# Kernel tuning notes

Hardware: AMD Instinct MI355X
Metric: run time of the kernel (lower is better)

## Reference

```python
import jax, jax.numpy as jnp
import numpy as np

IN_FEATS, N_HIDDEN, N_CLASSES = 128, 256, 32
N0, N1, B = 614400, 40960, 4096
F0, F1 = 15, 10
BN_EPS = 1e-5


def setup_inputs() -> dict:
    key = jax.random.key(0)
    ks = jax.random.split(key, 20)
    s = 0.02
    inp = {
        "x": jax.random.uniform(ks[0], (N0, IN_FEATS), jnp.float32) * 10.0,
        "nbr0": jax.random.randint(ks[1], (N1, F0), 0, N0, jnp.int32),
        "nbr1": jax.random.randint(ks[2], (B, F1), 0, N1, jnp.int32),
        # layer0: SAGEConv(128->256, 'pool')
        "W_pool": jax.random.normal(ks[3], (IN_FEATS, IN_FEATS), jnp.float32) * s,
        "b_pool": jnp.zeros((IN_FEATS,), jnp.float32),
        "W_self0": jax.random.normal(ks[4], (N_HIDDEN, IN_FEATS), jnp.float32) * s,
        "W_neigh0": jax.random.normal(ks[5], (N_HIDDEN, IN_FEATS), jnp.float32) * s,
        "b0": jnp.zeros((N_HIDDEN,), jnp.float32),
        # BatchNorm1d(n_hidden)
        "gamma0": jnp.ones((N_HIDDEN,), jnp.float32),
        "beta0": jnp.zeros((N_HIDDEN,), jnp.float32),
        # layer1: SAGEConv(256->32, 'lstm'); torch LSTM gate order i,f,g,o
        "W_ih": jax.random.normal(ks[6], (4 * N_HIDDEN, N_HIDDEN), jnp.float32) * s,
        "W_hh": jax.random.normal(ks[7], (4 * N_HIDDEN, N_HIDDEN), jnp.float32) * s,
        "b_ih": jnp.zeros((4 * N_HIDDEN,), jnp.float32),
        "b_hh": jnp.zeros((4 * N_HIDDEN,), jnp.float32),
        "W_self1": jax.random.normal(ks[8], (N_CLASSES, N_HIDDEN), jnp.float32) * s,
        "W_neigh1": jax.random.normal(ks[9], (N_CLASSES, N_HIDDEN), jnp.float32) * s,
        "b1": jnp.zeros((N_CLASSES,), jnp.float32),
    }
    return inp


def _lstm_agg(seq, W_ih, W_hh, b_ih, b_hh):
    # seq: [B, K, H]; run LSTM over K neighbor steps, return final hidden [B, H]
    Bsz, _, H = seq.shape
    xs = jnp.swapaxes(seq, 0, 1)  # [K, B, H]

    def step(carry, x_t):
        h_t, c_t = carry
        g = x_t @ W_ih.T + b_ih + h_t @ W_hh.T + b_hh  # [B, 4H]
        i, f, gg, o = jnp.split(g, 4, axis=-1)
        c = jax.nn.sigmoid(f) * c_t + jax.nn.sigmoid(i) * jnp.tanh(gg)
        h = jax.nn.sigmoid(o) * jnp.tanh(c)
        return (h, c), None

    init = (jnp.zeros((Bsz, H), seq.dtype), jnp.zeros((Bsz, H), seq.dtype))
    (hT, _), _ = jax.lax.scan(step, init, xs)
    return hT


def reference(x, nbr0, nbr1, W_pool, b_pool, W_self0, W_neigh0, b0,
              gamma0, beta0, W_ih, W_hh, b_ih, b_hh, W_self1, W_neigh1, b1):
    n1 = nbr0.shape[0]
    b = nbr1.shape[0]
    h = jnp.log(x + 1.0)  # [N0, in_feats]

    # --- layer 0: SAGEConv 'pool' ---
    hp = jax.nn.relu(h @ W_pool.T + b_pool)           # [N0, in_feats]
    h_neigh = jnp.max(hp[nbr0], axis=1)               # [N1, in_feats]
    h0 = h[:n1] @ W_self0.T + h_neigh @ W_neigh0.T + b0  # [N1, n_hidden]

    # BN (training stats) + relu (dropout p=0)
    mu = jnp.mean(h0, axis=0)
    var = jnp.var(h0, axis=0)
    h0 = (h0 - mu) * jax.lax.rsqrt(var + BN_EPS) * gamma0 + beta0
    h0 = jax.nn.relu(h0)

    # --- layer 1: SAGEConv 'lstm' ---
    seq = h0[nbr1]                                    # [B, F1, n_hidden]
    h_neigh1 = _lstm_agg(seq, W_ih, W_hh, b_ih, b_hh)  # [B, n_hidden]
    out = h0[:b] @ W_self1.T + h_neigh1 @ W_neigh1.T + b1  # [B, n_classes]
    return out
```

## Files before the change

### kernel.cpp

```cpp
#include <hip/hip_runtime.h>

#define N0v 614400
#define N1v 40960
#define BATCHv 4096

typedef __attribute__((ext_vector_type(8))) short short8;
typedef __attribute__((ext_vector_type(4))) float floatx4;

static __device__ __forceinline__ float flog1p(float v) { return __logf(v + 1.0f); }
static __device__ __forceinline__ float sigf(float v) { return 1.0f / (1.0f + __expf(-v)); }
static __device__ __forceinline__ float tanhfast(float v) {
    return 1.0f - 2.0f / (__expf(2.0f * v) + 1.0f);
}
static __device__ __forceinline__ unsigned short f2bf(float f) {
    union { float f; unsigned u; } v; v.f = f;
    unsigned r = v.u + 0x7FFFu + ((v.u >> 16) & 1u);
    return (unsigned short)(r >> 16);
}
static __device__ __forceinline__ float bf2f(unsigned short u) {
    return __uint_as_float(((unsigned)u) << 16);
}

__global__ __launch_bounds__(256) void cvt_weights_kernel(
    const float* __restrict__ Wp, const float* __restrict__ Ws0,
    const float* __restrict__ Wn0, const float* __restrict__ Wih,
    const float* __restrict__ Whh, const float* __restrict__ bih,
    const float* __restrict__ bhh,
    unsigned short* __restrict__ Wpb, unsigned short* __restrict__ Ws0b,
    unsigned short* __restrict__ Wn0b, unsigned short* __restrict__ Wihb,
    unsigned short* __restrict__ Whhb, float* __restrict__ bsum)
{
    const int g = blockIdx.x * 256 + threadIdx.x;
    if (g < 16384)            Wpb[g] = f2bf(Wp[g]);
    else if (g < 49152)       Ws0b[g - 16384] = f2bf(Ws0[g - 16384]);
    else if (g < 81920)       Wn0b[g - 49152] = f2bf(Wn0[g - 49152]);
    else if (g < 344064)      Wihb[g - 81920] = f2bf(Wih[g - 81920]);
    else if (g < 606208)      Whhb[g - 344064] = f2bf(Whh[g - 344064]);
    else if (g < 607232) { const int i = g - 606208; bsum[i] = bih[i] + bhh[i]; }
}

__global__ __launch_bounds__(256) void pool_max_kernel(
    const float* __restrict__ x, const int* __restrict__ nbr0,
    const unsigned short* __restrict__ Wpb, const float* __restrict__ bp,
    unsigned short* __restrict__ hnb)
{
    __shared__ unsigned short smem[64 * 72 + 128 * 72];
    __shared__ unsigned red[512];
    __shared__ int nodes[64];
    unsigned short* aT = smem;
    unsigned short* wT = smem + 64 * 72;

    const int tid = threadIdx.x;
    const size_t base = (size_t)blockIdx.x * 60;
    if (tid < 64) nodes[tid] = (tid < 60) ? nbr0[base + tid] : 0;
    for (int i = tid; i < 512; i += 256) red[i] = 0u;

    const int lane = tid & 63, wv = tid >> 6;
    const int ml = lane & 15, q = lane >> 4, qk = q * 8;

    floatx4 acc[8];
#pragma unroll
    for (int ct = 0; ct < 8; ++ct) acc[ct] = (floatx4){0.f, 0.f, 0.f, 0.f};

    for (int kc = 0; kc < 2; ++kc) {
        __syncthreads();
        for (int i = tid; i < 512; i += 256) {
            const int row = i >> 3, seg = i & 7;
            short8 o = {0, 0, 0, 0, 0, 0, 0, 0};
            if (row < 60) {
                const float* s = x + (size_t)nodes[row] * 128 + kc * 64 + seg * 8;
                const float4 f0 = *(const float4*)s;
                const float4 f1 = *(const float4*)(s + 4);
                o[0] = (short)f2bf(flog1p(f0.x)); o[1] = (short)f2bf(flog1p(f0.y));
                o[2] = (short)f2bf(flog1p(f0.z)); o[3] = (short)f2bf(flog1p(f0.w));
                o[4] = (short)f2bf(flog1p(f1.x)); o[5] = (short)f2bf(flog1p(f1.y));
                o[6] = (short)f2bf(flog1p(f1.z)); o[7] = (short)f2bf(flog1p(f1.w));
            }
            *(short8*)&aT[row * 72 + seg * 8] = o;
        }
        for (int i = tid; i < 1024; i += 256) {
            const int row = i >> 3, seg = i & 7;
            *(short8*)&wT[row * 72 + seg * 8] =
                *(const short8*)&Wpb[(size_t)row * 128 + kc * 64 + seg * 8];
        }
        __syncthreads();
#pragma unroll
        for (int k0 = 0; k0 < 64; k0 += 32) {
            const short8 a = *(const short8*)&aT[(wv * 16 + ml) * 72 + k0 + qk];
#pragma unroll
            for (int ct = 0; ct < 8; ++ct) {
                const short8 b = *(const short8*)&wT[(ct * 16 + ml) * 72 + k0 + qk];
                acc[ct] = __builtin_amdgcn_mfma_f32_16x16x32_bf16(a, b, acc[ct], 0, 0, 0);
            }
        }
    }
    __syncthreads();
#pragma unroll
    for (int ct = 0; ct < 8; ++ct) {
        const int col = ct * 16 + ml;
        const float bb = bp[col];
#pragma unroll
        for (int r = 0; r < 4; ++r) {
            const int row = wv * 16 + q * 4 + r;
            if (row < 60) {
                const float v = fmaxf(acc[ct][r] + bb, 0.0f);
                atomicMax(&red[(row / 15) * 128 + col], __float_as_uint(v));
            }
        }
    }
    __syncthreads();
    for (int i = tid; i < 512; i += 256)
        hnb[(size_t)blockIdx.x * 512 + i] = f2bf(__uint_as_float(red[i]));
}

__global__ __launch_bounds__(256) void h0_kernel(
    const float* __restrict__ x, const unsigned short* __restrict__ hnb,
    const unsigned short* __restrict__ Ws0b, const unsigned short* __restrict__ Wn0b,
    const float* __restrict__ b0, unsigned short* __restrict__ h0bf,
    float* __restrict__ bn_sum, float* __restrict__ bn_sq)
{
    __shared__ unsigned short smem[64 * 72 + 128 * 72];
    unsigned short* aT = smem;
    unsigned short* wT = smem + 64 * 72;

    const int tid = threadIdx.x;
    const int m0 = blockIdx.x * 64, c0 = blockIdx.y * 128;
    const int lane = tid & 63, wv = tid >> 6;
    const int ml = lane & 15, q = lane >> 4, qk = q * 8;

    floatx4 acc[8];
#pragma unroll
    for (int ct = 0; ct < 8; ++ct) acc[ct] = (floatx4){0.f, 0.f, 0.f, 0.f};

    for (int kc = 0; kc < 4; ++kc) {
        __syncthreads();
        for (int i = tid; i < 512; i += 256) {
            const int row = i >> 3, seg = i & 7;
            const int k = kc * 64 + seg * 8;
            if (kc < 2) {
                const float* s = x + (size_t)(m0 + row) * 128 + k;
                const float4 f0 = *(const float4*)s;
                const float4 f1 = *(const float4*)(s + 4);
                short8 o;
                o[0] = (short)f2bf(flog1p(f0.x)); o[1] = (short)f2bf(flog1p(f0.y));
                o[2] = (short)f2bf(flog1p(f0.z)); o[3] = (short)f2bf(flog1p(f0.w));
                o[4] = (short)f2bf(flog1p(f1.x)); o[5] = (short)f2bf(flog1p(f1.y));
                o[6] = (short)f2bf(flog1p(f1.z)); o[7] = (short)f2bf(flog1p(f1.w));
                *(short8*)&aT[row * 72 + seg * 8] = o;
            } else {
                *(short8*)&aT[row * 72 + seg * 8] =
                    *(const short8*)&hnb[(size_t)(m0 + row) * 128 + (k - 128)];
            }
        }
        for (int i = tid; i < 1024; i += 256) {
            const int row = i >> 3, seg = i & 7;
            const int k = kc * 64 + seg * 8;
            const size_t cg = (size_t)(c0 + row);
            *(short8*)&wT[row * 72 + seg * 8] = (kc < 2)
                ? *(const short8*)&Ws0b[cg * 128 + k]
                : *(const short8*)&Wn0b[cg * 128 + (k - 128)];
        }
        __syncthreads();
#pragma unroll
        for (int k0 = 0; k0 < 64; k0 += 32) {
            const short8 a = *(const short8*)&aT[(wv * 16 + ml) * 72 + k0 + qk];
#pragma unroll
            for (int ct = 0; ct < 8; ++ct) {
                const short8 b = *(const short8*)&wT[(ct * 16 + ml) * 72 + k0 + qk];
                acc[ct] = __builtin_amdgcn_mfma_f32_16x16x32_bf16(a, b, acc[ct], 0, 0, 0);
            }
        }
    }
    __syncthreads();
    float* scr = (float*)smem;
#pragma unroll
    for (int ct = 0; ct < 8; ++ct) {
        const int col = ct * 16 + ml, cg = c0 + col;
        const float bb = b0[cg];
        float s = 0.f, sq = 0.f;
#pragma unroll
        for (int r = 0; r < 4; ++r) {
            const int row = wv * 16 + q * 4 + r;
            const float v = acc[ct][r] + bb;
            h0bf[(size_t)(m0 + row) * 256 + cg] = f2bf(v);
            s += v; sq += v * v;
        }
        scr[(wv * 4 + q) * 128 + col] = s;
        scr[2048 + (wv * 4 + q) * 128 + col] = sq;
    }
    __syncthreads();
    if (tid < 128) {
        float s = 0.f, sq = 0.f;
#pragma unroll
        for (int j = 0; j < 16; ++j) {
            s += scr[j * 128 + tid];
            sq += scr[2048 + j * 128 + tid];
        }
        atomicAdd(&bn_sum[c0 + tid], s);
        atomicAdd(&bn_sq[c0 + tid], sq);
    }
}

__global__ void bn_stats_kernel(const float* __restrict__ bn_sum, const float* __restrict__ bn_sq,
                                const float* __restrict__ gamma, const float* __restrict__ beta,
                                float* __restrict__ scale, float* __restrict__ shift)
{
    const int c = threadIdx.x;
    const float inv_n = 1.0f / (float)N1v;
    const float mu = bn_sum[c] * inv_n;
    const float var = bn_sq[c] * inv_n - mu * mu;
    const float rs = rsqrtf(var + 1e-5f);
    const float sc = rs * gamma[c];
    scale[c] = sc;
    shift[c] = beta[c] - mu * sc;
}

__global__ __launch_bounds__(256) void bn_apply_kernel(
    const unsigned short* __restrict__ h0bf, const float* __restrict__ scale,
    const float* __restrict__ shift, unsigned short* __restrict__ h0nbf)
{
    const int gid = blockIdx.x * 256 + threadIdx.x;
    const int c0 = (gid * 8) & 255;
    const short8 v = *(const short8*)&h0bf[(size_t)gid * 8];
    short8 o;
#pragma unroll
    for (int j = 0; j < 8; ++j) {
        const float f = bf2f((unsigned short)v[j]);
        o[j] = (short)f2bf(fmaxf(fmaf(f, scale[c0 + j], shift[c0 + j]), 0.0f));
    }
    *(short8*)&h0nbf[(size_t)gid * 8] = o;
}

__global__ __launch_bounds__(256) void lstm_step_kernel(
    const unsigned short* __restrict__ h0nbf, const int* __restrict__ nbr1,
    const unsigned short* __restrict__ hbprev, const unsigned short* __restrict__ Wihb,
    const unsigned short* __restrict__ Whhb, const float* __restrict__ bsum,
    float* __restrict__ cst, unsigned short* __restrict__ hb, int t)
{
    __shared__ unsigned short smem[64 * 72 + 128 * 72];
    __shared__ int nodes[64];
    unsigned short* aT = smem;
    unsigned short* wT = smem + 64 * 72;

    const int tid = threadIdx.x;
    const int m0 = blockIdx.x * 64, c0h = blockIdx.y * 32;
    const int lane = tid & 63, wv = tid >> 6;
    const int ml = lane & 15, q = lane >> 4, qk = q * 8;

    if (tid < 64) nodes[tid] = nbr1[(size_t)(m0 + tid) * 10 + t];

    floatx4 acc[8];
#pragma unroll
    for (int ct = 0; ct < 8; ++ct) acc[ct] = (floatx4){0.f, 0.f, 0.f, 0.f};

    const int kcN = (t == 0) ? 4 : 8;
    for (int kc = 0; kc < kcN; ++kc) {
        __syncthreads();
        for (int i = tid; i < 512; i += 256) {
            const int row = i >> 3, seg = i & 7;
            const int k = kc * 64 + seg * 8;
            *(short8*)&aT[row * 72 + seg * 8] = (kc < 4)
                ? *(const short8*)&h0nbf[(size_t)nodes[row] * 256 + k]
                : *(const short8*)&hbprev[(size_t)(m0 + row) * 256 + (k - 256)];
        }
        for (int i = tid; i < 1024; i += 256) {
            const int row = i >> 3, seg = i & 7;
            const int k = kc * 64 + seg * 8;
            const size_t wr = (size_t)((row >> 5) * 256 + c0h + (row & 31));
            *(short8*)&wT[row * 72 + seg * 8] = (kc < 4)
                ? *(const short8*)&Wihb[wr * 256 + k]
                : *(const short8*)&Whhb[wr * 256 + (k - 256)];
        }
        __syncthreads();
#pragma unroll
        for (int k0 = 0; k0 < 64; k0 += 32) {
            const short8 a = *(const short8*)&aT[(wv * 16 + ml) * 72 + k0 + qk];
#pragma unroll
            for (int ct = 0; ct < 8; ++ct) {
                const short8 b = *(const short8*)&wT[(ct * 16 + ml) * 72 + k0 + qk];
                acc[ct] = __builtin_amdgcn_mfma_f32_16x16x32_bf16(a, b, acc[ct], 0, 0, 0);
            }
        }
    }
#pragma unroll
    for (int hg = 0; hg < 2; ++hg) {
        const int hcol = hg * 16 + ml;
        const float bi = bsum[c0h + hcol];
        const float bf_ = bsum[256 + c0h + hcol];
        const float bg = bsum[512 + c0h + hcol];
        const float bo = bsum[768 + c0h + hcol];
#pragma unroll
        for (int r = 0; r < 4; ++r) {
            const int row = wv * 16 + q * 4 + r;
            const size_t idx = (size_t)(m0 + row) * 256 + c0h + hcol;
            const float gi = acc[hg][r] + bi;
            const float gf = acc[2 + hg][r] + bf_;
            const float gg = acc[4 + hg][r] + bg;
            const float go = acc[6 + hg][r] + bo;
            float c = sigf(gi) * tanhfast(gg);
            if (t > 0) c += sigf(gf) * cst[idx];
            cst[idx] = c;
            hb[idx] = f2bf(sigf(go) * tanhfast(c));
        }
    }
}

__global__ __launch_bounds__(256) void out_kernel(
    const unsigned short* __restrict__ h0nbf, const unsigned short* __restrict__ hTb,
    const float* __restrict__ Ws1, const float* __restrict__ Wn1,
    const float* __restrict__ b1, float* __restrict__ out)
{
    const int gid = blockIdx.x * 256 + threadIdx.x;
    const int row = gid >> 5, c = gid & 31;
    const unsigned short* a0 = h0nbf + (size_t)row * 256;
    const unsigned short* a1 = hTb + (size_t)row * 256;
    const float* w0 = Ws1 + (size_t)c * 256;
    const float* w1 = Wn1 + (size_t)c * 256;
    float s = b1[c];
#pragma unroll 4
    for (int k8 = 0; k8 < 32; ++k8) {
        const short8 av = *(const short8*)&a0[k8 * 8];
        const short8 bv = *(const short8*)&a1[k8 * 8];
        const float4 wa0 = *(const float4*)&w0[k8 * 8];
        const float4 wa1 = *(const float4*)&w0[k8 * 8 + 4];
        const float4 wb0 = *(const float4*)&w1[k8 * 8];
        const float4 wb1 = *(const float4*)&w1[k8 * 8 + 4];
        s += bf2f((unsigned short)av[0]) * wa0.x + bf2f((unsigned short)av[1]) * wa0.y;
        s += bf2f((unsigned short)av[2]) * wa0.z + bf2f((unsigned short)av[3]) * wa0.w;
        s += bf2f((unsigned short)av[4]) * wa1.x + bf2f((unsigned short)av[5]) * wa1.y;
        s += bf2f((unsigned short)av[6]) * wa1.z + bf2f((unsigned short)av[7]) * wa1.w;
        s += bf2f((unsigned short)bv[0]) * wb0.x + bf2f((unsigned short)bv[1]) * wb0.y;
        s += bf2f((unsigned short)bv[2]) * wb0.z + bf2f((unsigned short)bv[3]) * wb0.w;
        s += bf2f((unsigned short)bv[4]) * wb1.x + bf2f((unsigned short)bv[5]) * wb1.y;
        s += bf2f((unsigned short)bv[6]) * wb1.z + bf2f((unsigned short)bv[7]) * wb1.w;
    }
    out[gid] = s;
}

extern "C" void kernel_launch(void* const* d_in, const int* in_sizes, int n_in,
                              void* d_out, int out_size, void* d_ws, size_t ws_size,
                              hipStream_t stream)
{
    const float* x        = (const float*)d_in[0];
    const int*   nbr0     = (const int*)d_in[1];
    const int*   nbr1     = (const int*)d_in[2];
    const float* W_pool   = (const float*)d_in[3];
    const float* b_pool   = (const float*)d_in[4];
    const float* W_self0  = (const float*)d_in[5];
    const float* W_neigh0 = (const float*)d_in[6];
    const float* b0       = (const float*)d_in[7];
    const float* gamma0   = (const float*)d_in[8];
    const float* beta0    = (const float*)d_in[9];
    const float* W_ih     = (const float*)d_in[10];
    const float* W_hh     = (const float*)d_in[11];
    const float* b_ih     = (const float*)d_in[12];
    const float* b_hh     = (const float*)d_in[13];
    const float* W_self1  = (const float*)d_in[14];
    const float* W_neigh1 = (const float*)d_in[15];
    const float* b1       = (const float*)d_in[16];
    float* out = (float*)d_out;

    char* ws = (char*)d_ws;
    unsigned short* h0bf  = (unsigned short*)(ws);
    unsigned short* hnb   = (unsigned short*)(ws + 20971520);
    unsigned short* h0nbf = (unsigned short*)(ws + 31457280);
    float*          cst   = (float*)(ws + 52428800);
    unsigned short* hb0   = (unsigned short*)(ws + 56623104);
    unsigned short* hb1   = (unsigned short*)(ws + 58720256);
    unsigned short* Wpb   = (unsigned short*)(ws + 60817408);
    unsigned short* Ws0b  = (unsigned short*)(ws + 60850176);
    unsigned short* Wn0b  = (unsigned short*)(ws + 60915712);
    unsigned short* Wihb  = (unsigned short*)(ws + 60981248);
    unsigned short* Whhb  = (unsigned short*)(ws + 61505536);
    float*          bsum  = (float*)(ws + 62029824);
    float*          bn_sum   = (float*)(ws + 62033920);
    float*          bn_sq    = (float*)(ws + 62034944);
    float*          bn_scale = (float*)(ws + 62035968);
    float*          bn_shift = (float*)(ws + 62036992);

    hipMemsetAsync(bn_sum, 0, 2048, stream);

    cvt_weights_kernel<<<2372, 256, 0, stream>>>(W_pool, W_self0, W_neigh0, W_ih, W_hh,
                                                 b_ih, b_hh, Wpb, Ws0b, Wn0b, Wihb, Whhb, bsum);
    pool_max_kernel<<<N1v / 4, 256, 0, stream>>>(x, nbr0, Wpb, b_pool, hnb);
    h0_kernel<<<dim3(N1v / 64, 2), 256, 0, stream>>>(x, hnb, Ws0b, Wn0b, b0,
                                                     h0bf, bn_sum, bn_sq);
    bn_stats_kernel<<<1, 256, 0, stream>>>(bn_sum, bn_sq, gamma0, beta0, bn_scale, bn_shift);
    bn_apply_kernel<<<(N1v * 256 / 8) / 256, 256, 0, stream>>>(h0bf, bn_scale, bn_shift, h0nbf);

    for (int t = 0; t < 10; ++t) {
        const unsigned short* hp = (t & 1) ? hb1 : hb0;
        unsigned short*       hn = (t & 1) ? hb0 : hb1;
        lstm_step_kernel<<<dim3(BATCHv / 64, 8), 256, 0, stream>>>(
            h0nbf, nbr1, hp, Wihb, Whhb, bsum, cst, hn, t);
    }
    out_kernel<<<(BATCHv * 32) / 256, 256, 0, stream>>>(h0nbf, hb0, W_self1, W_neigh1, b1, out);
}
```

Measured before the change: 777.1 us.

## Fuse BN apply and LSTM steps into one cooperative persistent kernel

Replaces the BN-apply kernel and the ten per-timestep LSTM launches with a single cooperative kernel. A grid-wide sync separates the BN-apply phase from the LSTM phase and each timestep from the next. The aim is to remove eleven kernel launch gaps and tail effects. In exchange, the kernel now pays grid-barrier costs and is limited to 512 co-resident blocks, and the launch fails if those blocks cannot all be resident.

```diff
diff --git a/kernel.cpp b/kernel.cpp
--- a/kernel.cpp
+++ b/kernel.cpp
@@ -1,4 +1,7 @@
 #include <hip/hip_runtime.h>
+#include <hip/hip_cooperative_groups.h>
+
+namespace cg = cooperative_groups;
 
 #define N0v 614400
 #define N1v 40960
@@ -215,28 +218,16 @@
     shift[c] = beta[c] - mu * sc;
 }
 
-__global__ __launch_bounds__(256) void bn_apply_kernel(
-    const unsigned short* __restrict__ h0bf, const float* __restrict__ scale,
-    const float* __restrict__ shift, unsigned short* __restrict__ h0nbf)
-{
-    const int gid = blockIdx.x * 256 + threadIdx.x;
-    const int c0 = (gid * 8) & 255;
-    const short8 v = *(const short8*)&h0bf[(size_t)gid * 8];
-    short8 o;
-#pragma unroll
-    for (int j = 0; j < 8; ++j) {
-        const float f = bf2f((unsigned short)v[j]);
-        o[j] = (short)f2bf(fmaxf(fmaf(f, scale[c0 + j], shift[c0 + j]), 0.0f));
-    }
-    *(short8*)&h0nbf[(size_t)gid * 8] = o;
-}
-
-__global__ __launch_bounds__(256) void lstm_step_kernel(
-    const unsigned short* __restrict__ h0nbf, const int* __restrict__ nbr1,
-    const unsigned short* __restrict__ hbprev, const unsigned short* __restrict__ Wihb,
+__global__ __launch_bounds__(256) void lstm_coop_kernel(
+    const unsigned short* __restrict__ h0bf, unsigned short* __restrict__ h0nbf,
+    const int* __restrict__ nbr1, const unsigned short* __restrict__ Wihb,
     const unsigned short* __restrict__ Whhb, const float* __restrict__ bsum,
-    float* __restrict__ cst, unsigned short* __restrict__ hb, int t)
-{
+    const float* __restrict__ bn_scale, const float* __restrict__ bn_shift,
+    float* __restrict__ cst, unsigned short* __restrict__ hb0,
+    unsigned short* __restrict__ hb1)
+{
+    cg::grid_group gg = cg::this_grid();
+
     __shared__ unsigned short smem[64 * 72 + 128 * 72];
     __shared__ int nodes[64];
     unsigned short* aT = smem;
@@ -247,61 +238,83 @@
     const int lane = tid & 63, wv = tid >> 6;
     const int ml = lane & 15, q = lane >> 4, qk = q * 8;
 
-    if (tid < 64) nodes[tid] = nbr1[(size_t)(m0 + tid) * 10 + t];
-
-    floatx4 acc[8];
-#pragma unroll
-    for (int ct = 0; ct < 8; ++ct) acc[ct] = (floatx4){0.f, 0.f, 0.f, 0.f};
-
-    const int kcN = (t == 0) ? 4 : 8;
-    for (int kc = 0; kc < kcN; ++kc) {
-        __syncthreads();
-        for (int i = tid; i < 512; i += 256) {
-            const int row = i >> 3, seg = i & 7;
-            const int k = kc * 64 + seg * 8;
-            *(short8*)&aT[row * 72 + seg * 8] = (kc < 4)
-                ? *(const short8*)&h0nbf[(size_t)nodes[row] * 256 + k]
-                : *(const short8*)&hbprev[(size_t)(m0 + row) * 256 + (k - 256)];
-        }
-        for (int i = tid; i < 1024; i += 256) {
-            const int row = i >> 3, seg = i & 7;
-            const int k = kc * 64 + seg * 8;
-            const size_t wr = (size_t)((row >> 5) * 256 + c0h + (row & 31));
-            *(short8*)&wT[row * 72 + seg * 8] = (kc < 4)
-                ? *(const short8*)&Wihb[wr * 256 + k]
-                : *(const short8*)&Whhb[wr * 256 + (k - 256)];
-        }
-        __syncthreads();
-#pragma unroll
-        for (int k0 = 0; k0 < 64; k0 += 32) {
-            const short8 a = *(const short8*)&aT[(wv * 16 + ml) * 72 + k0 + qk];
-#pragma unroll
-            for (int ct = 0; ct < 8; ++ct) {
-                const short8 b = *(const short8*)&wT[(ct * 16 + ml) * 72 + k0 + qk];
-                acc[ct] = __builtin_amdgcn_mfma_f32_16x16x32_bf16(a, b, acc[ct], 0, 0, 0);
-            }
-        }
-    }
-#pragma unroll
-    for (int hg = 0; hg < 2; ++hg) {
-        const int hcol = hg * 16 + ml;
-        const float bi = bsum[c0h + hcol];
-        const float bf_ = bsum[256 + c0h + hcol];
-        const float bg = bsum[512 + c0h + hcol];
-        const float bo = bsum[768 + c0h + hcol];
-#pragma unroll
-        for (int r = 0; r < 4; ++r) {
-            const int row = wv * 16 + q * 4 + r;
-            const size_t idx = (size_t)(m0 + row) * 256 + c0h + hcol;
-            const float gi = acc[hg][r] + bi;
-            const float gf = acc[2 + hg][r] + bf_;
-            const float gg = acc[4 + hg][r] + bg;
-            const float go = acc[6 + hg][r] + bo;
-            float c = sigf(gi) * tanhfast(gg);
-            if (t > 0) c += sigf(gf) * cst[idx];
-            cst[idx] = c;
-            hb[idx] = f2bf(sigf(go) * tanhfast(c));
-        }
+    {
+        const int gblk = blockIdx.y * gridDim.x + blockIdx.x;
+        for (int gid = gblk * 256 + tid; gid < N1v * 32; gid += 512 * 256) {
+            const int c0 = (gid * 8) & 255;
+            const short8 v = *(const short8*)&h0bf[(size_t)gid * 8];
+            short8 o;
+#pragma unroll
+            for (int j = 0; j < 8; ++j) {
+                const float f = bf2f((unsigned short)v[j]);
+                o[j] = (short)f2bf(fmaxf(fmaf(f, bn_scale[c0 + j], bn_shift[c0 + j]), 0.0f));
+            }
+            *(short8*)&h0nbf[(size_t)gid * 8] = o;
+        }
+    }
+    gg.sync();
+
+    for (int t = 0; t < 10; ++t) {
+        const unsigned short* hbprev = (t & 1) ? hb1 : hb0;
+        unsigned short*       hbn    = (t & 1) ? hb0 : hb1;
+
+        if (tid < 64) nodes[tid] = nbr1[(size_t)(m0 + tid) * 10 + t];
+
+        floatx4 acc[8];
+#pragma unroll
+        for (int ct = 0; ct < 8; ++ct) acc[ct] = (floatx4){0.f, 0.f, 0.f, 0.f};
+
+        const int kcN = (t == 0) ? 4 : 8;
+        for (int kc = 0; kc < kcN; ++kc) {
+            __syncthreads();
+            for (int i = tid; i < 512; i += 256) {
+                const int row = i >> 3, seg = i & 7;
+                const int k = kc * 64 + seg * 8;
+                *(short8*)&aT[row * 72 + seg * 8] = (kc < 4)
+                    ? *(const short8*)&h0nbf[(size_t)nodes[row] * 256 + k]
+                    : *(const short8*)&hbprev[(size_t)(m0 + row) * 256 + (k - 256)];
+            }
+            for (int i = tid; i < 1024; i += 256) {
+                const int row = i >> 3, seg = i & 7;
+                const int k = kc * 64 + seg * 8;
+                const size_t wr = (size_t)((row >> 5) * 256 + c0h + (row & 31));
+                *(short8*)&wT[row * 72 + seg * 8] = (kc < 4)
+                    ? *(const short8*)&Wihb[wr * 256 + k]
+                    : *(const short8*)&Whhb[wr * 256 + (k - 256)];
+            }
+            __syncthreads();
+#pragma unroll
+            for (int k0 = 0; k0 < 64; k0 += 32) {
+                const short8 a = *(const short8*)&aT[(wv * 16 + ml) * 72 + k0 + qk];
+#pragma unroll
+                for (int ct = 0; ct < 8; ++ct) {
+                    const short8 b = *(const short8*)&wT[(ct * 16 + ml) * 72 + k0 + qk];
+                    acc[ct] = __builtin_amdgcn_mfma_f32_16x16x32_bf16(a, b, acc[ct], 0, 0, 0);
+                }
+            }
+        }
+#pragma unroll
+        for (int hg = 0; hg < 2; ++hg) {
+            const int hcol = hg * 16 + ml;
+            const float bi = bsum[c0h + hcol];
+            const float bf_ = bsum[256 + c0h + hcol];
+            const float bg = bsum[512 + c0h + hcol];
+            const float bo = bsum[768 + c0h + hcol];
+#pragma unroll
+            for (int r = 0; r < 4; ++r) {
+                const int row = wv * 16 + q * 4 + r;
+                const size_t idx = (size_t)(m0 + row) * 256 + c0h + hcol;
+                const float gi = acc[0 + hg][r] + bi;
+                const float gf = acc[2 + hg][r] + bf_;
+                const float gg2 = acc[4 + hg][r] + bg;
+                const float go = acc[6 + hg][r] + bo;
+                float c = sigf(gi) * tanhfast(gg2);
+                if (t > 0) c += sigf(gf) * cst[idx];
+                cst[idx] = c;
+                hbn[idx] = f2bf(sigf(go) * tanhfast(c));
+            }
+        }
+        if (t < 9) gg.sync();
     }
 }
 
@@ -386,13 +399,16 @@
     h0_kernel<<<dim3(N1v / 64, 2), 256, 0, stream>>>(x, hnb, Ws0b, Wn0b, b0,
                                                      h0bf, bn_sum, bn_sq);
     bn_stats_kernel<<<1, 256, 0, stream>>>(bn_sum, bn_sq, gamma0, beta0, bn_scale, bn_shift);
-    bn_apply_kernel<<<(N1v * 256 / 8) / 256, 256, 0, stream>>>(h0bf, bn_scale, bn_shift, h0nbf);
-
-    for (int t = 0; t < 10; ++t) {
-        const unsigned short* hp = (t & 1) ? hb1 : hb0;
-        unsigned short*       hn = (t & 1) ? hb0 : hb1;
-        lstm_step_kernel<<<dim3(BATCHv / 64, 8), 256, 0, stream>>>(
-            h0nbf, nbr1, hp, Wihb, Whhb, bsum, cst, hn, t);
+
+    {
+        void* args[] = {
+            (void*)&h0bf, (void*)&h0nbf, (void*)&nbr1, (void*)&Wihb, (void*)&Whhb,
+            (void*)&bsum, (void*)&bn_scale, (void*)&bn_shift,
+            (void*)&cst, (void*)&hb0, (void*)&hb1
+        };
+        hipLaunchCooperativeKernel((const void*)lstm_coop_kernel,
+                                   dim3(BATCHv / 64, 8), dim3(256),
+                                   args, 0, stream);
     }
     out_kernel<<<(BATCHv * 32) / 256, 256, 0, stream>>>(h0nbf, hb0, W_self1, W_neigh1, b1, out);
 }
```

Measured after the change: 1.349 ms. +73.6%, slower.

## Read MFMA B operands directly from global weights and stage full-K A tiles

Applied to the files above, without the earlier changes.

In the pool, h0 and LSTM-step kernels, the weight tiles are no longer staged through LDS. Each lane now loads its bf16 B fragments straight from global or cache, and the whole K extent of the activation tile is staged in LDS once. This removes the per-K-chunk barriers and the LDS weight copies. The cost is more global/L2 traffic for weights across waves and larger LDS allocations for A, which may reduce occupancy.

```diff
diff --git a/kernel.cpp b/kernel.cpp
--- a/kernel.cpp
+++ b/kernel.cpp
@@ -44,11 +44,9 @@
     const unsigned short* __restrict__ Wpb, const float* __restrict__ bp,
     unsigned short* __restrict__ hnb)
 {
-    __shared__ unsigned short smem[64 * 72 + 128 * 72];
+    __shared__ unsigned short aT[64 * 136];
     __shared__ unsigned red[512];
     __shared__ int nodes[64];
-    unsigned short* aT = smem;
-    unsigned short* wT = smem + 64 * 72;
 
     const int tid = threadIdx.x;
     const size_t base = (size_t)blockIdx.x * 60;
@@ -58,43 +56,37 @@
     const int lane = tid & 63, wv = tid >> 6;
     const int ml = lane & 15, q = lane >> 4, qk = q * 8;
 
+    __syncthreads();
+    for (int i = tid; i < 1024; i += 256) {
+        const int row = i >> 4, seg = i & 15;
+        short8 o = {0, 0, 0, 0, 0, 0, 0, 0};
+        if (row < 60) {
+            const float* s = x + (size_t)nodes[row] * 128 + seg * 8;
+            const float4 f0 = *(const float4*)s;
+            const float4 f1 = *(const float4*)(s + 4);
+            o[0] = (short)f2bf(flog1p(f0.x)); o[1] = (short)f2bf(flog1p(f0.y));
+            o[2] = (short)f2bf(flog1p(f0.z)); o[3] = (short)f2bf(flog1p(f0.w));
+            o[4] = (short)f2bf(flog1p(f1.x)); o[5] = (short)f2bf(flog1p(f1.y));
+            o[6] = (short)f2bf(flog1p(f1.z)); o[7] = (short)f2bf(flog1p(f1.w));
+        }
+        *(short8*)&aT[row * 136 + seg * 8] = o;
+    }
+    __syncthreads();
+
     floatx4 acc[8];
 #pragma unroll
     for (int ct = 0; ct < 8; ++ct) acc[ct] = (floatx4){0.f, 0.f, 0.f, 0.f};
 
-    for (int kc = 0; kc < 2; ++kc) {
-        __syncthreads();
-        for (int i = tid; i < 512; i += 256) {
-            const int row = i >> 3, seg = i & 7;
-            short8 o = {0, 0, 0, 0, 0, 0, 0, 0};
-            if (row < 60) {
-                const float* s = x + (size_t)nodes[row] * 128 + kc * 64 + seg * 8;
-                const float4 f0 = *(const float4*)s;
-                const float4 f1 = *(const float4*)(s + 4);
-                o[0] = (short)f2bf(flog1p(f0.x)); o[1] = (short)f2bf(flog1p(f0.y));
-                o[2] = (short)f2bf(flog1p(f0.z)); o[3] = (short)f2bf(flog1p(f0.w));
-                o[4] = (short)f2bf(flog1p(f1.x)); o[5] = (short)f2bf(flog1p(f1.y));
-                o[6] = (short)f2bf(flog1p(f1.z)); o[7] = (short)f2bf(flog1p(f1.w));
-            }
-            *(short8*)&aT[row * 72 + seg * 8] = o;
-        }
-        for (int i = tid; i < 1024; i += 256) {
-            const int row = i >> 3, seg = i & 7;
-            *(short8*)&wT[row * 72 + seg * 8] =
-                *(const short8*)&Wpb[(size_t)row * 128 + kc * 64 + seg * 8];
-        }
-        __syncthreads();
-#pragma unroll
-        for (int k0 = 0; k0 < 64; k0 += 32) {
-            const short8 a = *(const short8*)&aT[(wv * 16 + ml) * 72 + k0 + qk];
-#pragma unroll
-            for (int ct = 0; ct < 8; ++ct) {
-                const short8 b = *(const short8*)&wT[(ct * 16 + ml) * 72 + k0 + qk];
-                acc[ct] = __builtin_amdgcn_mfma_f32_16x16x32_bf16(a, b, acc[ct], 0, 0, 0);
-            }
-        }
-    }
-    __syncthreads();
+#pragma unroll
+    for (int k0 = 0; k0 < 128; k0 += 32) {
+        const short8 a = *(const short8*)&aT[(wv * 16 + ml) * 136 + k0 + qk];
+#pragma unroll
+        for (int ct = 0; ct < 8; ++ct) {
+            const short8 b = *(const short8*)&Wpb[(size_t)(ct * 16 + ml) * 128 + k0 + qk];
+            acc[ct] = __builtin_amdgcn_mfma_f32_16x16x32_bf16(a, b, acc[ct], 0, 0, 0);
+        }
+    }
+
 #pragma unroll
     for (int ct = 0; ct < 8; ++ct) {
         const int col = ct * 16 + ml;
@@ -119,60 +111,57 @@
     const float* __restrict__ b0, unsigned short* __restrict__ h0bf,
     float* __restrict__ bn_sum, float* __restrict__ bn_sq)
 {
-    __shared__ unsigned short smem[64 * 72 + 128 * 72];
-    unsigned short* aT = smem;
-    unsigned short* wT = smem + 64 * 72;
+    __shared__ unsigned short aT[64 * 264];
 
     const int tid = threadIdx.x;
     const int m0 = blockIdx.x * 64, c0 = blockIdx.y * 128;
     const int lane = tid & 63, wv = tid >> 6;
     const int ml = lane & 15, q = lane >> 4, qk = q * 8;
 
+    for (int i = tid; i < 2048; i += 256) {
+        const int row = i >> 5, seg = i & 31;
+        if (seg < 16) {
+            const float* s = x + (size_t)(m0 + row) * 128 + seg * 8;
+            const float4 f0 = *(const float4*)s;
+            const float4 f1 = *(const float4*)(s + 4);
+            short8 o;
+            o[0] = (short)f2bf(flog1p(f0.x)); o[1] = (short)f2bf(flog1p(f0.y));
+            o[2] = (short)f2bf(flog1p(f0.z)); o[3] = (short)f2bf(flog1p(f0.w));
+            o[4] = (short)f2bf(flog1p(f1.x)); o[5] = (short)f2bf(flog1p(f1.y));
+            o[6] = (short)f2bf(flog1p(f1.z)); o[7] = (short)f2bf(flog1p(f1.w));
+            *(short8*)&aT[row * 264 + seg * 8] = o;
+        } else {
+            *(short8*)&aT[row * 264 + seg * 8] =
+                *(const short8*)&hnb[(size_t)(m0 + row) * 128 + (seg - 16) * 8];
+        }
+    }
+    __syncthreads();
+
     floatx4 acc[8];
 #pragma unroll
     for (int ct = 0; ct < 8; ++ct) acc[ct] = (floatx4){0.f, 0.f, 0.f, 0.f};
 
-    for (int kc = 0; kc < 4; ++kc) {
-        __syncthreads();
-        for (int i = tid; i < 512; i += 256) {
-            const int row = i >> 3, seg = i & 7;
-            const int k = kc * 64 + seg * 8;
-            if (kc < 2) {
-                const float* s = x + (size_t)(m0 + row) * 128 + k;
-                const float4 f0 = *(const float4*)s;
-                const float4 f1 = *(const float4*)(s + 4);
-                short8 o;
-                o[0] = (short)f2bf(flog1p(f0.x)); o[1] = (short)f2bf(flog1p(f0.y));
-                o[2] = (short)f2bf(flog1p(f0.z)); o[3] = (short)f2bf(flog1p(f0.w));
-                o[4] = (short)f2bf(flog1p(f1.x)); o[5] = (short)f2bf(flog1p(f1.y));
-                o[6] = (short)f2bf(flog1p(f1.z)); o[7] = (short)f2bf(flog1p(f1.w));
-                *(short8*)&aT[row * 72 + seg * 8] = o;
-            } else {
-                *(short8*)&aT[row * 72 + seg * 8] =
-                    *(const short8*)&hnb[(size_t)(m0 + row) * 128 + (k - 128)];
-            }
-        }
-        for (int i = tid; i < 1024; i += 256) {
-            const int row = i >> 3, seg = i & 7;
-            const int k = kc * 64 + seg * 8;
-            const size_t cg = (size_t)(c0 + row);
-            *(short8*)&wT[row * 72 + seg * 8] = (kc < 2)
-                ? *(const short8*)&Ws0b[cg * 128 + k]
-                : *(const short8*)&Wn0b[cg * 128 + (k - 128)];
-        }
-        __syncthreads();
-#pragma unroll
-        for (int k0 = 0; k0 < 64; k0 += 32) {
-            const short8 a = *(const short8*)&aT[(wv * 16 + ml) * 72 + k0 + qk];
-#pragma unroll
-            for (int ct = 0; ct < 8; ++ct) {
-                const short8 b = *(const short8*)&wT[(ct * 16 + ml) * 72 + k0 + qk];
-                acc[ct] = __builtin_amdgcn_mfma_f32_16x16x32_bf16(a, b, acc[ct], 0, 0, 0);
-            }
-        }
-    }
-    __syncthreads();
-    float* scr = (float*)smem;
+#pragma unroll
+    for (int kk = 0; kk < 4; ++kk) {
+        const short8 a = *(const short8*)&aT[(wv * 16 + ml) * 264 + kk * 32 + qk];
+#pragma unroll
+        for (int ct = 0; ct < 8; ++ct) {
+            const short8 b = *(const short8*)&Ws0b[(size_t)(c0 + ct * 16 + ml) * 128 + kk * 32 + qk];
+            acc[ct] = __builtin_amdgcn_mfma_f32_16x16x32_bf16(a, b, acc[ct], 0, 0, 0);
+        }
+    }
+#pragma unroll
+    for (int kk = 0; kk < 4; ++kk) {
+        const short8 a = *(const short8*)&aT[(wv * 16 + ml) * 264 + 128 + kk * 32 + qk];
+#pragma unroll
+        for (int ct = 0; ct < 8; ++ct) {
+            const short8 b = *(const short8*)&Wn0b[(size_t)(c0 + ct * 16 + ml) * 128 + kk * 32 + qk];
+            acc[ct] = __builtin_amdgcn_mfma_f32_16x16x32_bf16(a, b, acc[ct], 0, 0, 0);
+        }
+    }
+    __syncthreads();
+
+    float* scr = (float*)aT;
 #pragma unroll
     for (int ct = 0; ct < 8; ++ct) {
         const int col = ct * 16 + ml, cg = c0 + col;
@@ -237,10 +226,8 @@
     const unsigned short* __restrict__ Whhb, const float* __restrict__ bsum,
     float* __restrict__ cst, unsigned short* __restrict__ hb, int t)
 {
-    __shared__ unsigned short smem[64 * 72 + 128 * 72];
+    __shared__ unsigned short aT[64 * 264];
     __shared__ int nodes[64];
-    unsigned short* aT = smem;
-    unsigned short* wT = smem + 64 * 72;
 
     const int tid = threadIdx.x;
     const int m0 = blockIdx.x * 64, c0h = blockIdx.y * 32;
@@ -249,39 +236,50 @@
 
     if (tid < 64) nodes[tid] = nbr1[(size_t)(m0 + tid) * 10 + t];
 
+    size_t wroff[8];
+#pragma unroll
+    for (int ct = 0; ct < 8; ++ct)
+        wroff[ct] = (size_t)((ct >> 1) * 256 + c0h + (ct & 1) * 16 + ml) * 256;
+
     floatx4 acc[8];
 #pragma unroll
     for (int ct = 0; ct < 8; ++ct) acc[ct] = (floatx4){0.f, 0.f, 0.f, 0.f};
 
-    const int kcN = (t == 0) ? 4 : 8;
-    for (int kc = 0; kc < kcN; ++kc) {
+    __syncthreads();
+    for (int i = tid; i < 2048; i += 256) {
+        const int row = i >> 5, seg = i & 31;
+        *(short8*)&aT[row * 264 + seg * 8] =
+            *(const short8*)&h0nbf[(size_t)nodes[row] * 256 + seg * 8];
+    }
+    __syncthreads();
+#pragma unroll
+    for (int kk = 0; kk < 8; ++kk) {
+        const short8 a = *(const short8*)&aT[(wv * 16 + ml) * 264 + kk * 32 + qk];
+#pragma unroll
+        for (int ct = 0; ct < 8; ++ct) {
+            const short8 b = *(const short8*)&Wihb[wroff[ct] + kk * 32 + qk];
+            acc[ct] = __builtin_amdgcn_mfma_f32_16x16x32_bf16(a, b, acc[ct], 0, 0, 0);
+        }
+    }
+    if (t > 0) {
         __syncthreads();
-        for (int i = tid; i < 512; i += 256) {
-            const int row = i >> 3, seg = i & 7;
-            const int k = kc * 64 + seg * 8;
-            *(short8*)&aT[row * 72 + seg * 8] = (kc < 4)
-                ? *(const short8*)&h0nbf[(size_t)nodes[row] * 256 + k]
-                : *(const short8*)&hbprev[(size_t)(m0 + row) * 256 + (k - 256)];
-        }
-        for (int i = tid; i < 1024; i += 256) {
-            const int row = i >> 3, seg = i & 7;
-            const int k = kc * 64 + seg * 8;
-            const size_t wr = (size_t)((row >> 5) * 256 + c0h + (row & 31));
-            *(short8*)&wT[row * 72 + seg * 8] = (kc < 4)
-                ? *(const short8*)&Wihb[wr * 256 + k]
-                : *(const short8*)&Whhb[wr * 256 + (k - 256)];
+        for (int i = tid; i < 2048; i += 256) {
+            const int row = i >> 5, seg = i & 31;
+            *(short8*)&aT[row * 264 + seg * 8] =
+                *(const short8*)&hbprev[(size_t)(m0 + row) * 256 + seg * 8];
         }
         __syncthreads();
 #pragma unroll
-        for (int k0 = 0; k0 < 64; k0 += 32) {
-            const short8 a = *(const short8*)&aT[(wv * 16 + ml) * 72 + k0 + qk];
+        for (int kk = 0; kk < 8; ++kk) {
+            const short8 a = *(const short8*)&aT[(wv * 16 + ml) * 264 + kk * 32 + qk];
 #pragma unroll
             for (int ct = 0; ct < 8; ++ct) {
-                const short8 b = *(const short8*)&wT[(ct * 16 + ml) * 72 + k0 + qk];
+                const short8 b = *(const short8*)&Whhb[wroff[ct] + kk * 32 + qk];
                 acc[ct] = __builtin_amdgcn_mfma_f32_16x16x32_bf16(a, b, acc[ct], 0, 0, 0);
             }
         }
     }
+
 #pragma unroll
     for (int hg = 0; hg < 2; ++hg) {
         const int hcol = hg * 16 + ml;
@@ -293,7 +291,7 @@
         for (int r = 0; r < 4; ++r) {
             const int row = wv * 16 + q * 4 + r;
             const size_t idx = (size_t)(m0 + row) * 256 + c0h + hcol;
-            const float gi = acc[hg][r] + bi;
+            const float gi = acc[0 + hg][r] + bi;
             const float gf = acc[2 + hg][r] + bf_;
             const float gg = acc[4 + hg][r] + bg;
             const float go = acc[6 + hg][r] + bo;
```

New measurement: 1.038 ms. 33.6% more time.

## Compute pool projection densely over all nodes, then gather-max; fold BN stats into apply

Applied to the files above, without the earlier changes.

Instead of recomputing the pool projection for each of the 614400 gathered neighbor rows, the pool MLP now runs once over all N0 nodes as a dense MFMA GEMM and stores a bf16 result. A separate gather kernel then takes the max over the 15 neighbors, reading about 256 bytes per row. The separate BN stats launch is folded into bn_apply, where every block recomputes scale and shift into shared memory. The new path only runs when the workspace holds the extra 150MB buffer, and it trades duplicated compute for extra memory traffic.

```diff
diff --git a/kernel.cpp b/kernel.cpp
--- a/kernel.cpp
+++ b/kernel.cpp
@@ -37,6 +37,85 @@
     else if (g < 344064)      Wihb[g - 81920] = f2bf(Wih[g - 81920]);
     else if (g < 606208)      Whhb[g - 344064] = f2bf(Whh[g - 344064]);
     else if (g < 607232) { const int i = g - 606208; bsum[i] = bih[i] + bhh[i]; }
+}
+
+__global__ __launch_bounds__(256) void pool_dense_kernel(
+    const float* __restrict__ x, const unsigned short* __restrict__ Wpb,
+    const float* __restrict__ bp, unsigned short* __restrict__ hpb)
+{
+    __shared__ unsigned short smem[64 * 72 + 128 * 72];
+    unsigned short* aT = smem;
+    unsigned short* wT = smem + 64 * 72;
+
+    const int tid = threadIdx.x;
+    const int m0 = blockIdx.x * 64;
+    const int lane = tid & 63, wv = tid >> 6;
+    const int ml = lane & 15, q = lane >> 4, qk = q * 8;
+
+    floatx4 acc[8];
+#pragma unroll
+    for (int ct = 0; ct < 8; ++ct) acc[ct] = (floatx4){0.f, 0.f, 0.f, 0.f};
+
+    for (int kc = 0; kc < 2; ++kc) {
+        __syncthreads();
+        for (int i = tid; i < 512; i += 256) {
+            const int row = i >> 3, seg = i & 7;
+            const float* s = x + (size_t)(m0 + row) * 128 + kc * 64 + seg * 8;
+            const float4 f0 = *(const float4*)s;
+            const float4 f1 = *(const float4*)(s + 4);
+            short8 o;
+            o[0] = (short)f2bf(flog1p(f0.x)); o[1] = (short)f2bf(flog1p(f0.y));
+            o[2] = (short)f2bf(flog1p(f0.z)); o[3] = (short)f2bf(flog1p(f0.w));
+            o[4] = (short)f2bf(flog1p(f1.x)); o[5] = (short)f2bf(flog1p(f1.y));
+            o[6] = (short)f2bf(flog1p(f1.z)); o[7] = (short)f2bf(flog1p(f1.w));
+            *(short8*)&aT[row * 72 + seg * 8] = o;
+        }
+        for (int i = tid; i < 1024; i += 256) {
+            const int row = i >> 3, seg = i & 7;
+            *(short8*)&wT[row * 72 + seg * 8] =
+                *(const short8*)&Wpb[(size_t)row * 128 + kc * 64 + seg * 8];
+        }
+        __syncthreads();
+#pragma unroll
+        for (int k0 = 0; k0 < 64; k0 += 32) {
+            const short8 a = *(const short8*)&aT[(wv * 16 + ml) * 72 + k0 + qk];
+#pragma unroll
+            for (int ct = 0; ct < 8; ++ct) {
+                const short8 b = *(const short8*)&wT[(ct * 16 + ml) * 72 + k0 + qk];
+                acc[ct] = __builtin_amdgcn_mfma_f32_16x16x32_bf16(a, b, acc[ct], 0, 0, 0);
+            }
+        }
+    }
+#pragma unroll
+    for (int ct = 0; ct < 8; ++ct) {
+        const int col = ct * 16 + ml;
+        const float bb = bp[col];
+#pragma unroll
+        for (int r = 0; r < 4; ++r) {
+            const int row = wv * 16 + q * 4 + r;
+            hpb[(size_t)(m0 + row) * 128 + col] = f2bf(fmaxf(acc[ct][r] + bb, 0.0f));
+        }
+    }
+}
+
+__global__ __launch_bounds__(256) void pool_gather_kernel(
+    const unsigned short* __restrict__ hpb, const int* __restrict__ nbr0,
+    unsigned short* __restrict__ hnb)
+{
+    const int g = blockIdx.x * 256 + threadIdx.x;
+    const int node = g >> 6, lp = g & 63;
+    const unsigned* hp32 = (const unsigned*)hpb;
+    float mlo = 0.0f, mhi = 0.0f;
+#pragma unroll
+    for (int j = 0; j < 15; ++j) {
+        const int idx = nbr0[node * 15 + j];
+        const unsigned v = hp32[(size_t)idx * 64 + lp];
+        mlo = fmaxf(mlo, bf2f((unsigned short)(v & 0xffffu)));
+        mhi = fmaxf(mhi, bf2f((unsigned short)(v >> 16)));
+    }
+    const unsigned lo = __float_as_uint(mlo) >> 16;
+    const unsigned hi = __float_as_uint(mhi) & 0xffff0000u;
+    ((unsigned*)hnb)[(size_t)node * 64 + lp] = hi | lo;
 }
 
 __global__ __launch_bounds__(256) void pool_max_kernel(
@@ -201,32 +280,31 @@
     }
 }
 
-__global__ void bn_stats_kernel(const float* __restrict__ bn_sum, const float* __restrict__ bn_sq,
-                                const float* __restrict__ gamma, const float* __restrict__ beta,
-                                float* __restrict__ scale, float* __restrict__ shift)
-{
-    const int c = threadIdx.x;
-    const float inv_n = 1.0f / (float)N1v;
-    const float mu = bn_sum[c] * inv_n;
-    const float var = bn_sq[c] * inv_n - mu * mu;
-    const float rs = rsqrtf(var + 1e-5f);
-    const float sc = rs * gamma[c];
-    scale[c] = sc;
-    shift[c] = beta[c] - mu * sc;
-}
-
 __global__ __launch_bounds__(256) void bn_apply_kernel(
-    const unsigned short* __restrict__ h0bf, const float* __restrict__ scale,
-    const float* __restrict__ shift, unsigned short* __restrict__ h0nbf)
-{
-    const int gid = blockIdx.x * 256 + threadIdx.x;
+    const unsigned short* __restrict__ h0bf, const float* __restrict__ bn_sum,
+    const float* __restrict__ bn_sq, const float* __restrict__ gamma,
+    const float* __restrict__ beta, unsigned short* __restrict__ h0nbf)
+{
+    __shared__ float sc[256], sh[256];
+    const int tid = threadIdx.x;
+    {
+        const float inv_n = 1.0f / (float)N1v;
+        const float mu = bn_sum[tid] * inv_n;
+        const float var = bn_sq[tid] * inv_n - mu * mu;
+        const float rs = rsqrtf(var + 1e-5f);
+        const float s = rs * gamma[tid];
+        sc[tid] = s;
+        sh[tid] = beta[tid] - mu * s;
+    }
+    __syncthreads();
+    const int gid = blockIdx.x * 256 + tid;
     const int c0 = (gid * 8) & 255;
     const short8 v = *(const short8*)&h0bf[(size_t)gid * 8];
     short8 o;
 #pragma unroll
     for (int j = 0; j < 8; ++j) {
         const float f = bf2f((unsigned short)v[j]);
-        o[j] = (short)f2bf(fmaxf(fmaf(f, scale[c0 + j], shift[c0 + j]), 0.0f));
+        o[j] = (short)f2bf(fmaxf(fmaf(f, sc[c0 + j], sh[c0 + j]), 0.0f));
     }
     *(short8*)&h0nbf[(size_t)gid * 8] = o;
 }
@@ -293,7 +371,7 @@
         for (int r = 0; r < 4; ++r) {
             const int row = wv * 16 + q * 4 + r;
             const size_t idx = (size_t)(m0 + row) * 256 + c0h + hcol;
-            const float gi = acc[hg][r] + bi;
+            const float gi = acc[0 + hg][r] + bi;
             const float gf = acc[2 + hg][r] + bf_;
             const float gg = acc[4 + hg][r] + bg;
             const float go = acc[6 + hg][r] + bo;
@@ -361,32 +439,60 @@
     float* out = (float*)d_out;
 
     char* ws = (char*)d_ws;
-    unsigned short* h0bf  = (unsigned short*)(ws);
-    unsigned short* hnb   = (unsigned short*)(ws + 20971520);
-    unsigned short* h0nbf = (unsigned short*)(ws + 31457280);
-    float*          cst   = (float*)(ws + 52428800);
-    unsigned short* hb0   = (unsigned short*)(ws + 56623104);
-    unsigned short* hb1   = (unsigned short*)(ws + 58720256);
-    unsigned short* Wpb   = (unsigned short*)(ws + 60817408);
-    unsigned short* Ws0b  = (unsigned short*)(ws + 60850176);
-    unsigned short* Wn0b  = (unsigned short*)(ws + 60915712);
-    unsigned short* Wihb  = (unsigned short*)(ws + 60981248);
-    unsigned short* Whhb  = (unsigned short*)(ws + 61505536);
-    float*          bsum  = (float*)(ws + 62029824);
-    float*          bn_sum   = (float*)(ws + 62033920);
-    float*          bn_sq    = (float*)(ws + 62034944);
-    float*          bn_scale = (float*)(ws + 62035968);
-    float*          bn_shift = (float*)(ws + 62036992);
+    const size_t NEED_BIG = 168990720;
+    const bool big = (ws_size >= NEED_BIG);
+
+    unsigned short *h0bf, *hnb, *h0nbf, *hb0, *hb1, *Wpb, *Ws0b, *Wn0b, *Wihb, *Whhb, *hpb;
+    float *cst, *bsum, *bn_sum, *bn_sq;
+
+    if (big) {
+        hnb   = (unsigned short*)(ws);
+        hpb   = (unsigned short*)(ws + 10485760);
+        h0bf  = (unsigned short*)(ws + 10485760);
+        h0nbf = (unsigned short*)(ws + 31457280);
+        cst   = (float*)         (ws + 52428800);
+        hb0   = (unsigned short*)(ws + 56623104);
+        hb1   = (unsigned short*)(ws + 58720256);
+        Wpb   = (unsigned short*)(ws + 167772160);
+        Ws0b  = (unsigned short*)(ws + 167804928);
+        Wn0b  = (unsigned short*)(ws + 167870464);
+        Wihb  = (unsigned short*)(ws + 167936000);
+        Whhb  = (unsigned short*)(ws + 168460288);
+        bsum  = (float*)         (ws + 168984576);
+        bn_sum= (float*)         (ws + 168988672);
+        bn_sq = (float*)         (ws + 168989696);
+    } else {
+        h0bf  = (unsigned short*)(ws);
+        hnb   = (unsigned short*)(ws + 20971520);
+        h0nbf = (unsigned short*)(ws + 31457280);
+        cst   = (float*)         (ws + 52428800);
+        hb0   = (unsigned short*)(ws + 56623104);
+        hb1   = (unsigned short*)(ws + 58720256);
+        Wpb   = (unsigned short*)(ws + 60817408);
+        Ws0b  = (unsigned short*)(ws + 60850176);
+        Wn0b  = (unsigned short*)(ws + 60915712);
+        Wihb  = (unsigned short*)(ws + 60981248);
+        Whhb  = (unsigned short*)(ws + 61505536);
+        bsum  = (float*)         (ws + 62029824);
+        bn_sum= (float*)         (ws + 62033920);
+        bn_sq = (float*)         (ws + 62034944);
+        hpb   = 0;
+    }
 
     hipMemsetAsync(bn_sum, 0, 2048, stream);
 
     cvt_weights_kernel<<<2372, 256, 0, stream>>>(W_pool, W_self0, W_neigh0, W_ih, W_hh,
                                                  b_ih, b_hh, Wpb, Ws0b, Wn0b, Wihb, Whhb, bsum);
-    pool_max_kernel<<<N1v / 4, 256, 0, stream>>>(x, nbr0, Wpb, b_pool, hnb);
+    if (big) {
+        pool_dense_kernel<<<N0v / 64, 256, 0, stream>>>(x, Wpb, b_pool, hpb);
+        pool_gather_kernel<<<(N1v * 64) / 256, 256, 0, stream>>>(hpb, nbr0, hnb);
+    } else {
+        pool_max_kernel<<<N1v / 4, 256, 0, stream>>>(x, nbr0, Wpb, b_pool, hnb);
+    }
     h0_kernel<<<dim3(N1v / 64, 2), 256, 0, stream>>>(x, hnb, Ws0b, Wn0b, b0,
                                                      h0bf, bn_sum, bn_sq);
-    bn_stats_kernel<<<1, 256, 0, stream>>>(bn_sum, bn_sq, gamma0, beta0, bn_scale, bn_shift);
-    bn_apply_kernel<<<(N1v * 256 / 8) / 256, 256, 0, stream>>>(h0bf, bn_scale, bn_shift, h0nbf);
+    bn_apply_kernel<<<(N1v * 256 / 8) / 256, 256, 0, stream>>>(h0bf, bn_sum, bn_sq,
+                                                               gamma0, beta0, h0nbf);
 
     for (int t = 0; t < 10; ++t) {
         const unsigned short* hp = (t & 1) ? hb1 : hb0;
```

After: 797.0 us. +2.6%, slower.
